# Kernel optimization log

Hardware: AMD Instinct MI355X
Metric: run time of the kernel (lower is better)

Reference implementation:

```python
import jax, jax.numpy as jnp
import numpy as np

D_MODEL = 768
N_HEADS = 12
HEAD = 64
B, T = 2, 2048


def setup_inputs() -> dict:
    key = jax.random.key(0)
    k1, k2, k3 = jax.random.split(key, 3)
    x = jax.random.normal(k1, (B, T, D_MODEL), dtype=jnp.float32)
    W1 = jax.random.normal(k2, (3 * D_MODEL, D_MODEL), dtype=jnp.float32) * (1.0 / np.sqrt(D_MODEL))
    b1 = jnp.zeros((3 * D_MODEL,), dtype=jnp.float32)
    W2 = jax.random.normal(k3, (D_MODEL, D_MODEL), dtype=jnp.float32) * (1.0 / np.sqrt(D_MODEL))
    b2 = jnp.zeros((D_MODEL,), dtype=jnp.float32)
    return {"x": x, "W1": W1, "b1": b1, "W2": W2, "b2": b2}


def reference(x, W1, b1, W2, b2):
    Bx, Tx, C = x.shape
    qkv = jnp.einsum('btc,fc->btf', x, W1) + b1            # (B,T,3C)
    q, k, v = jnp.split(qkv, 3, axis=-1)
    # (B,T,H,Dh) -> (B,H,T,Dh)
    q = q.reshape(Bx, Tx, N_HEADS, HEAD).transpose(0, 2, 1, 3)
    k = k.reshape(Bx, Tx, N_HEADS, HEAD).transpose(0, 2, 1, 3)
    v = v.reshape(Bx, Tx, N_HEADS, HEAD).transpose(0, 2, 1, 3)
    scale = 1.0 / np.sqrt(HEAD)
    scores = jnp.einsum('bhqd,bhkd->bhqk', q, k) * scale   # (B,H,T,T)
    causal = jnp.tril(jnp.ones((Tx, Tx), dtype=bool))
    scores = jnp.where(causal, scores, jnp.finfo(scores.dtype).min)
    attn = jax.nn.softmax(scores, axis=-1)
    o = jnp.einsum('bhqk,bhkd->bhqd', attn, v)             # (B,H,T,Dh)
    o = o.transpose(0, 2, 1, 3).reshape(Bx, Tx, C)
    return jnp.einsum('btc,fc->btf', o, W2) + b2
```

## Files before the change

### kernel.cpp

```cpp
#include <hip/hip_runtime.h>


typedef float f32x4 __attribute__((ext_vector_type(4)));
typedef __bf16 bf16x8 __attribute__((ext_vector_type(8)));

#define D_MODEL 768
#define F3 2304
#define NHEADS 12
#define HEAD 64
#define BB 2
#define TT 2048
#define MROWS (BB*TT)
#define KDIM 768
#define LOG2E 1.44269504f
#define NX (MROWS*D_MODEL)
#define NW1 (F3*KDIM)
#define NW2 (D_MODEL*KDIM)

__device__ __forceinline__ unsigned short f2bf(float f) {
    unsigned int u = __float_as_uint(f);
    u += 0x7fffu + ((u >> 16) & 1u);
    return (unsigned short)(u >> 16);
}
__device__ __forceinline__ unsigned int pack2bf(float a, float b) {
    unsigned int ua = __float_as_uint(a), ub = __float_as_uint(b);
    ua += 0x7fffu + ((ua >> 16) & 1u);
    ub += 0x7fffu + ((ub >> 16) & 1u);
    return (ua >> 16) | (ub & 0xffff0000u);
}

__device__ __forceinline__ void async_copy16(unsigned short* lds, const unsigned short* g) {
    __builtin_amdgcn_global_load_lds(
        (const __attribute__((address_space(1))) unsigned int*)(const void*)g,
        (__attribute__((address_space(3))) unsigned int*)(void*)lds,
        16, 0, 0);
}

__global__ void prep(const float* __restrict__ x, const float* __restrict__ W1,
                     const float* __restrict__ W2, unsigned short* __restrict__ xb,
                     unsigned short* __restrict__ w1b, unsigned short* __restrict__ w2b) {
    const int i4 = (blockIdx.x * blockDim.x + threadIdx.x) * 4;
    const float* src; unsigned short* dst; int off;
    if (i4 < NX)                { src = x;  dst = xb;  off = i4; }
    else if (i4 < NX + NW1)     { src = W1; dst = w1b; off = i4 - NX; }
    else if (i4 < NX + NW1 + NW2) { src = W2; dst = w2b; off = i4 - NX - NW1; }
    else return;
    float4 v = *(const float4*)(src + off);
    uint2 o;
    o.x = pack2bf(v.x, v.y);
    o.y = pack2bf(v.z, v.w);
    *(uint2*)(dst + off) = o;
}

__global__ __launch_bounds__(256, 4) void gemm1(
    const unsigned short* __restrict__ A, const unsigned short* __restrict__ Bw,
    const float* __restrict__ bias, int K,
    unsigned short* __restrict__ Qb, unsigned short* __restrict__ Kb,
    unsigned short* __restrict__ VT)
{
    __shared__ unsigned short As[128*64];
    __shared__ unsigned short Bs[128*64];
    const int tid  = threadIdx.x;
    const int wave = tid >> 6;
    const int lane = tid & 63;
    const int quad = lane >> 4;
    const int l16  = lane & 15;
    const int m0 = blockIdx.x * 128;
    const int n0 = blockIdx.y * 128;
    const int wm = (wave >> 1) * 64;
    const int wn = (wave & 1) * 64;

    f32x4 acc[4][4] = {};

    const unsigned short* Ablk = A + (size_t)m0 * K;
    const unsigned short* Bblk = Bw + (size_t)n0 * K;
    const int srow = (lane >> 3);
    const int scol = ((lane & 7) ^ srow) * 8;

    for (int k0 = 0; k0 < K; k0 += 64) {
        #pragma unroll
        for (int q2 = 0; q2 < 4; ++q2) {
            int t = wave * 4 + q2;
            int row = t * 8 + srow;
            async_copy16(As + t * 512, Ablk + (size_t)row * K + k0 + scol);
            async_copy16(Bs + t * 512, Bblk + (size_t)row * K + k0 + scol);
        }
        asm volatile("s_waitcnt vmcnt(0)" ::: "memory");
        __syncthreads();

        #pragma unroll
        for (int kc2 = 0; kc2 < 2; ++kc2) {
            const int pos = ((kc2*4 + quad) ^ (l16 & 7)) * 8;
            bf16x8 a[4], b[4];
            #pragma unroll
            for (int i = 0; i < 4; ++i)
                a[i] = *(const bf16x8*)(As + (wm + i*16 + l16)*64 + pos);
            #pragma unroll
            for (int j = 0; j < 4; ++j)
                b[j] = *(const bf16x8*)(Bs + (wn + j*16 + l16)*64 + pos);
            #pragma unroll
            for (int i = 0; i < 4; ++i)
                #pragma unroll
                for (int j = 0; j < 4; ++j)
                    acc[i][j] = __builtin_amdgcn_mfma_f32_16x16x32_bf16(a[i], b[j], acc[i][j], 0, 0, 0);
        }
        __syncthreads();
    }

    const int seg = blockIdx.y / 6;
    if (seg < 2) {
        #pragma unroll
        for (int j = 0; j < 4; ++j) {
            const int n = n0 + wn + j*16 + l16;
            const float bv = bias[n];
            const int f = n - seg * 768;
            const int h = f >> 6, d = f & 63;
            #pragma unroll
            for (int i = 0; i < 4; ++i)
                #pragma unroll
                for (int r = 0; r < 4; ++r) {
                    const int m = m0 + wm + i*16 + quad*4 + r;
                    const int b = m >> 11, t = m & 2047;
                    const size_t idx = (((size_t)(b*NHEADS + h)) * TT + t) * HEAD + d;
                    const float v = acc[i][j][r] + bv;
                    if (seg == 0) Qb[idx] = f2bf(v * (0.125f * LOG2E));
                    else          Kb[idx] = f2bf(v);
                }
        }
    } else {
        #pragma unroll
        for (int j = 0; j < 4; ++j) {
            const int n = n0 + wn + j*16 + l16;
            const float bv = bias[n];
            const int f = n - 1536;
            const int h = f >> 6, d = f & 63;
            #pragma unroll
            for (int i = 0; i < 4; ++i) {
                const int m = m0 + wm + i*16 + quad*4;
                const int b = m >> 11, t = m & 2047;
                uint2 pk;
                pk.x = pack2bf(acc[i][j][0] + bv, acc[i][j][1] + bv);
                pk.y = pack2bf(acc[i][j][2] + bv, acc[i][j][3] + bv);
                *(uint2*)(VT + ((size_t)(b*NHEADS + h) * HEAD + d) * TT + t) = pk;
            }
        }
    }
}

__global__ __launch_bounds__(256, 4) void gemm2(
    const unsigned short* __restrict__ A, const unsigned short* __restrict__ Bw,
    const float* __restrict__ bias, int K, float* __restrict__ Cout)
{
    __shared__ unsigned short As[64*64];
    __shared__ unsigned short Bs[128*64];
    const int tid  = threadIdx.x;
    const int wave = tid >> 6;
    const int lane = tid & 63;
    const int quad = lane >> 4;
    const int l16  = lane & 15;
    const int m0 = blockIdx.x * 64;
    const int n0 = blockIdx.y * 128;
    const int wm = (wave >> 1) * 32;
    const int wn = (wave & 1) * 64;

    f32x4 acc[2][4] = {};

    const unsigned short* Ablk = A + (size_t)m0 * K;
    const unsigned short* Bblk = Bw + (size_t)n0 * K;
    const int srow = tid >> 3;
    const int scol = ((tid & 7) ^ (srow & 7)) * 8;

    for (int k0 = 0; k0 < K; k0 += 64) {
        #pragma unroll
        for (int i = 0; i < 2; ++i)
            async_copy16(As + i*2048 + tid*8,
                         Ablk + (size_t)(i*32 + srow) * K + k0 + scol);
        #pragma unroll
        for (int i = 0; i < 4; ++i)
            async_copy16(Bs + i*2048 + tid*8,
                         Bblk + (size_t)(i*32 + srow) * K + k0 + scol);
        asm volatile("s_waitcnt vmcnt(0)" ::: "memory");
        __syncthreads();

        #pragma unroll
        for (int kc2 = 0; kc2 < 2; ++kc2) {
            const int pos = ((kc2*4 + quad) ^ (l16 & 7)) * 8;
            bf16x8 a[2], b[4];
            #pragma unroll
            for (int i = 0; i < 2; ++i)
                a[i] = *(const bf16x8*)(As + (wm + i*16 + l16)*64 + pos);
            #pragma unroll
            for (int j = 0; j < 4; ++j)
                b[j] = *(const bf16x8*)(Bs + (wn + j*16 + l16)*64 + pos);
            #pragma unroll
            for (int i = 0; i < 2; ++i)
                #pragma unroll
                for (int j = 0; j < 4; ++j)
                    acc[i][j] = __builtin_amdgcn_mfma_f32_16x16x32_bf16(a[i], b[j], acc[i][j], 0, 0, 0);
        }
        __syncthreads();
    }

    #pragma unroll
    for (int j = 0; j < 4; ++j) {
        const int n = n0 + wn + j*16 + l16;
        const float bv = bias[n];
        #pragma unroll
        for (int i = 0; i < 2; ++i)
            #pragma unroll
            for (int r = 0; r < 4; ++r) {
                const int m = m0 + wm + i*16 + quad*4 + r;
                Cout[(size_t)m * D_MODEL + n] = acc[i][j][r] + bv;
            }
    }
}

__global__ __launch_bounds__(256, 2) void attn(
    const unsigned short* __restrict__ Qb, const unsigned short* __restrict__ Kb,
    const unsigned short* __restrict__ VT, unsigned short* __restrict__ Ob)
{
    __shared__ unsigned short Ks[128*64];
    __shared__ unsigned short Vt[64*128];
    __shared__ unsigned short Ps[4][16*128];

    const int tid  = threadIdx.x;
    const int wave = tid >> 6;
    const int lane = tid & 63;
    const int quad = lane >> 4;
    const int l16  = lane & 15;
    const int qt = (blockIdx.x + blockIdx.y) & 31;
    const int bh = blockIdx.y;
    const size_t hbase = (size_t)bh * TT * HEAD;
    const int qg = qt*64 + wave*16 + l16;

    bf16x8 qreg[2];
    {
        const unsigned short* qp = Qb + hbase + (size_t)qg * HEAD + quad*8;
        qreg[0] = *(const bf16x8*)(qp);
        qreg[1] = *(const bf16x8*)(qp + 32);
    }

    const int krow = tid >> 3;
    const int kchunk = ((tid & 7) ^ (krow & 7)) * 8;
    const int vrow = tid >> 4;
    const int vchunk = ((tid & 15) ^ vrow) * 8;

    f32x4 oacc[4] = {};
    float lst = 0.f;
    const int nkt = (qt >> 1) + 1;

    for (int kt = 0; kt < nkt; ++kt) {
        __syncthreads();

        const unsigned short* ksrc = Kb + hbase + (size_t)kt * 128 * HEAD;
        #pragma unroll
        for (int i = 0; i < 4; ++i)
            async_copy16(Ks + i*2048 + tid*8,
                         ksrc + (size_t)(i*32 + krow) * 64 + kchunk);
        #pragma unroll
        for (int i = 0; i < 4; ++i)
            async_copy16(Vt + i*2048 + tid*8,
                         VT + hbase + (size_t)(i*16 + vrow) * TT + kt*128 + vchunk);
        asm volatile("s_waitcnt vmcnt(0)" ::: "memory");
        __syncthreads();

        f32x4 s[8] = {};
        #pragma unroll
        for (int kc2 = 0; kc2 < 2; ++kc2) {
            bf16x8 bq = qreg[kc2];
            const int pos = ((kc2*4 + quad) ^ (l16 & 7)) * 8;
            #pragma unroll
            for (int nt = 0; nt < 8; ++nt) {
                bf16x8 ak = *(const bf16x8*)(Ks + (nt*16 + l16)*64 + pos);
                s[nt] = __builtin_amdgcn_mfma_f32_16x16x32_bf16(ak, bq, s[nt], 0, 0, 0);
            }
        }

        if (kt == nkt - 1) {
            const int kq = kt*128 + quad*4;
            #pragma unroll
            for (int nt = 0; nt < 8; ++nt)
                #pragma unroll
                for (int r = 0; r < 4; ++r)
                    if (kq + nt*16 + r > qg) s[nt][r] = -1e30f;
        }

        float rsum = 0.f;
        uint2 pck[8];
        #pragma unroll
        for (int nt = 0; nt < 8; ++nt) {
            const float p0 = exp2f(s[nt][0]);
            const float p1 = exp2f(s[nt][1]);
            const float p2 = exp2f(s[nt][2]);
            const float p3 = exp2f(s[nt][3]);
            rsum += (p0 + p1) + (p2 + p3);
            pck[nt].x = (__float_as_uint(p0) >> 16) | (__float_as_uint(p1) & 0xffff0000u);
            pck[nt].y = (__float_as_uint(p2) >> 16) | (__float_as_uint(p3) & 0xffff0000u);
        }
        rsum += __shfl_xor(rsum, 16);
        rsum += __shfl_xor(rsum, 32);
        lst += rsum;

        #pragma unroll
        for (int nt = 0; nt < 8; ++nt)
            *(uint2*)(&Ps[wave][l16*128 + ((nt*2 + (quad>>1)) ^ l16)*8 + (quad&1)*4]) = pck[nt];

        #pragma unroll
        for (int kc = 0; kc < 4; ++kc) {
            bf16x8 ap = *(const bf16x8*)(&Ps[wave][l16*128 + ((kc*4 + quad) ^ l16)*8]);
            const int vp = ((kc*4 + quad) ^ l16) * 8;
            #pragma unroll
            for (int dt = 0; dt < 4; ++dt) {
                bf16x8 bv = *(const bf16x8*)(Vt + (dt*16 + l16)*128 + vp);
                oacc[dt] = __builtin_amdgcn_mfma_f32_16x16x32_bf16(ap, bv, oacc[dt], 0, 0, 0);
            }
        }
    }

    const float linv = 1.0f / lst;
    float lr[4];
    #pragma unroll
    for (int r = 0; r < 4; ++r) lr[r] = __shfl(linv, quad*4 + r);
    const int b = bh / NHEADS, h = bh % NHEADS;
    #pragma unroll
    for (int r = 0; r < 4; ++r) {
        const int m = b * TT + qt*64 + wave*16 + quad*4 + r;
        #pragma unroll
        for (int dt = 0; dt < 4; ++dt)
            Ob[(size_t)m * D_MODEL + h*HEAD + dt*16 + l16] = f2bf(oacc[dt][r] * lr[r]);
    }
}

extern "C" void kernel_launch(void* const* d_in, const int* in_sizes, int n_in,
                              void* d_out, int out_size, void* d_ws, size_t ws_size,
                              hipStream_t stream) {
    const float* x  = (const float*)d_in[0];
    const float* W1 = (const float*)d_in[1];
    const float* b1 = (const float*)d_in[2];
    const float* W2 = (const float*)d_in[3];
    const float* b2 = (const float*)d_in[4];
    float* out = (float*)d_out;

    unsigned short* ws = (unsigned short*)d_ws;
    unsigned short* xb  = ws;
    unsigned short* w1b = xb  + (size_t)NX;
    unsigned short* w2b = w1b + (size_t)NW1;
    unsigned short* Qb  = w2b + (size_t)NW2;
    unsigned short* Kb  = Qb + (size_t)BB*NHEADS*TT*HEAD;
    unsigned short* VT  = Kb + (size_t)BB*NHEADS*TT*HEAD;
    unsigned short* Ob  = VT + (size_t)BB*NHEADS*TT*HEAD;

    prep<<<((NX + NW1 + NW2)/4 + 255)/256, 256, 0, stream>>>(x, W1, W2, xb, w1b, w2b);

    gemm1<<<dim3(MROWS/128, F3/128), 256, 0, stream>>>(
        xb, w1b, b1, KDIM, Qb, Kb, VT);

    attn<<<dim3(32, BB*NHEADS), 256, 0, stream>>>(Qb, Kb, VT, Ob);

    gemm2<<<dim3(MROWS/64, D_MODEL/128), 256, 0, stream>>>(
        Ob, w2b, b2, KDIM, out);
}
```

Baseline: 153.4 us.

## Balance causal attention by splitting long query tiles across paired blocks

Each attention block now handles a short query tile fully plus part of a long query tile, so every block processes roughly the same number of key tiles under the causal mask. Partial numerators and row sums for long tiles are accumulated with float atomics into zeroed workspace buffers, and a new fixup kernel normalises them and writes bf16 output. This targets the load imbalance where late query tiles did far more work than early ones. The cost is extra zeroing in prep, atomic traffic, and an additional kernel launch.

```diff
diff --git a/kernel.cpp b/kernel.cpp
--- a/kernel.cpp
+++ b/kernel.cpp
@@ -16,6 +16,10 @@
 #define NX (MROWS*D_MODEL)
 #define NW1 (F3*KDIM)
 #define NW2 (D_MODEL*KDIM)
+#define NHT 16
+#define NOF (BB*NHEADS*NHT*64*64)
+#define NLF (BB*NHEADS*NHT*64)
+#define NZF (NOF+NLF)
 
 __device__ __forceinline__ unsigned short f2bf(float f) {
     unsigned int u = __float_as_uint(f);
@@ -38,12 +42,18 @@
 
 __global__ void prep(const float* __restrict__ x, const float* __restrict__ W1,
                      const float* __restrict__ W2, unsigned short* __restrict__ xb,
-                     unsigned short* __restrict__ w1b, unsigned short* __restrict__ w2b) {
+                     unsigned short* __restrict__ w1b, unsigned short* __restrict__ w2b,
+                     float* __restrict__ zf) {
     const int i4 = (blockIdx.x * blockDim.x + threadIdx.x) * 4;
     const float* src; unsigned short* dst; int off;
-    if (i4 < NX)                { src = x;  dst = xb;  off = i4; }
-    else if (i4 < NX + NW1)     { src = W1; dst = w1b; off = i4 - NX; }
+    if (i4 < NX)                  { src = x;  dst = xb;  off = i4; }
+    else if (i4 < NX + NW1)       { src = W1; dst = w1b; off = i4 - NX; }
     else if (i4 < NX + NW1 + NW2) { src = W2; dst = w2b; off = i4 - NX - NW1; }
+    else if (i4 < NX + NW1 + NW2 + NZF) {
+        f32x4 z = {};
+        *(f32x4*)(zf + (i4 - (NX + NW1 + NW2))) = z;
+        return;
+    }
     else return;
     float4 v = *(const float4*)(src + off);
     uint2 o;
@@ -217,7 +227,8 @@
 
 __global__ __launch_bounds__(256, 2) void attn(
     const unsigned short* __restrict__ Qb, const unsigned short* __restrict__ Kb,
-    const unsigned short* __restrict__ VT, unsigned short* __restrict__ Ob)
+    const unsigned short* __restrict__ VT, unsigned short* __restrict__ Ob,
+    float* __restrict__ Of, float* __restrict__ Lf)
 {
     __shared__ unsigned short Ks[128*64];
     __shared__ unsigned short Vt[64*128];
@@ -228,107 +239,163 @@
     const int lane = tid & 63;
     const int quad = lane >> 4;
     const int l16  = lane & 15;
-    const int qt = (blockIdx.x + blockIdx.y) & 31;
-    const int bh = blockIdx.y;
+    const int j    = blockIdx.x;
+    const int bh   = blockIdx.y;
+    const int i    = j & 15;
+    const bool isA = (j < 16);
+    const int half = i >> 1;
+    const int split = 8 - half;
     const size_t hbase = (size_t)bh * TT * HEAD;
-    const int qg = qt*64 + wave*16 + l16;
-
-    bf16x8 qreg[2];
-    {
-        const unsigned short* qp = Qb + hbase + (size_t)qg * HEAD + quad*8;
-        qreg[0] = *(const bf16x8*)(qp);
-        qreg[1] = *(const bf16x8*)(qp + 32);
-    }
 
     const int krow = tid >> 3;
     const int kchunk = ((tid & 7) ^ (krow & 7)) * 8;
     const int vrow = tid >> 4;
     const int vchunk = ((tid & 15) ^ vrow) * 8;
 
-    f32x4 oacc[4] = {};
-    float lst = 0.f;
-    const int nkt = (qt >> 1) + 1;
-
-    for (int kt = 0; kt < nkt; ++kt) {
-        __syncthreads();
-
-        const unsigned short* ksrc = Kb + hbase + (size_t)kt * 128 * HEAD;
-        #pragma unroll
-        for (int i = 0; i < 4; ++i)
-            async_copy16(Ks + i*2048 + tid*8,
-                         ksrc + (size_t)(i*32 + krow) * 64 + kchunk);
-        #pragma unroll
-        for (int i = 0; i < 4; ++i)
-            async_copy16(Vt + i*2048 + tid*8,
-                         VT + hbase + (size_t)(i*16 + vrow) * TT + kt*128 + vchunk);
-        asm volatile("s_waitcnt vmcnt(0)" ::: "memory");
-        __syncthreads();
-
-        f32x4 s[8] = {};
-        #pragma unroll
-        for (int kc2 = 0; kc2 < 2; ++kc2) {
-            bf16x8 bq = qreg[kc2];
-            const int pos = ((kc2*4 + quad) ^ (l16 & 7)) * 8;
+    const int nseg = isA ? 2 : 1;
+    for (int segi = 0; segi < nseg; ++segi) {
+        int qt, kb, ke; bool full;
+        if (isA) {
+            if (segi == 0) { qt = i;      kb = 0;     ke = half + 1;  full = true;  }
+            else           { qt = 31 - i; kb = 0;     ke = split;     full = false; }
+        } else             { qt = 31 - i; kb = split; ke = 16 - half; full = false; }
+        const bool domask = (ke == (qt >> 1) + 1);
+        const int qg = qt*64 + wave*16 + l16;
+
+        bf16x8 qreg[2];
+        {
+            const unsigned short* qp = Qb + hbase + (size_t)qg * HEAD + quad*8;
+            qreg[0] = *(const bf16x8*)(qp);
+            qreg[1] = *(const bf16x8*)(qp + 32);
+        }
+
+        f32x4 oacc[4] = {};
+        float lst = 0.f;
+
+        for (int kt = kb; kt < ke; ++kt) {
+            __syncthreads();
+
+            const unsigned short* ksrc = Kb + hbase + (size_t)kt * 128 * HEAD;
+            #pragma unroll
+            for (int ii = 0; ii < 4; ++ii)
+                async_copy16(Ks + ii*2048 + tid*8,
+                             ksrc + (size_t)(ii*32 + krow) * 64 + kchunk);
+            #pragma unroll
+            for (int ii = 0; ii < 4; ++ii)
+                async_copy16(Vt + ii*2048 + tid*8,
+                             VT + hbase + (size_t)(ii*16 + vrow) * TT + kt*128 + vchunk);
+            asm volatile("s_waitcnt vmcnt(0)" ::: "memory");
+            __syncthreads();
+
+            f32x4 s[8] = {};
+            #pragma unroll
+            for (int kc2 = 0; kc2 < 2; ++kc2) {
+                bf16x8 bq = qreg[kc2];
+                const int pos = ((kc2*4 + quad) ^ (l16 & 7)) * 8;
+                #pragma unroll
+                for (int nt = 0; nt < 8; ++nt) {
+                    bf16x8 ak = *(const bf16x8*)(Ks + (nt*16 + l16)*64 + pos);
+                    s[nt] = __builtin_amdgcn_mfma_f32_16x16x32_bf16(ak, bq, s[nt], 0, 0, 0);
+                }
+            }
+
+            if (domask && kt == ke - 1) {
+                const int kq = kt*128 + quad*4;
+                #pragma unroll
+                for (int nt = 0; nt < 8; ++nt)
+                    #pragma unroll
+                    for (int r = 0; r < 4; ++r)
+                        if (kq + nt*16 + r > qg) s[nt][r] = -1e30f;
+            }
+
+            float rsum = 0.f;
+            uint2 pck[8];
             #pragma unroll
             for (int nt = 0; nt < 8; ++nt) {
-                bf16x8 ak = *(const bf16x8*)(Ks + (nt*16 + l16)*64 + pos);
-                s[nt] = __builtin_amdgcn_mfma_f32_16x16x32_bf16(ak, bq, s[nt], 0, 0, 0);
-            }
-        }
-
-        if (kt == nkt - 1) {
-            const int kq = kt*128 + quad*4;
+                const float p0 = exp2f(s[nt][0]);
+                const float p1 = exp2f(s[nt][1]);
+                const float p2 = exp2f(s[nt][2]);
+                const float p3 = exp2f(s[nt][3]);
+                rsum += (p0 + p1) + (p2 + p3);
+                pck[nt].x = (__float_as_uint(p0) >> 16) | (__float_as_uint(p1) & 0xffff0000u);
+                pck[nt].y = (__float_as_uint(p2) >> 16) | (__float_as_uint(p3) & 0xffff0000u);
+            }
+            rsum += __shfl_xor(rsum, 16);
+            rsum += __shfl_xor(rsum, 32);
+            lst += rsum;
+
             #pragma unroll
             for (int nt = 0; nt < 8; ++nt)
+                *(uint2*)(&Ps[wave][l16*128 + ((nt*2 + (quad>>1)) ^ l16)*8 + (quad&1)*4]) = pck[nt];
+
+            #pragma unroll
+            for (int kc = 0; kc < 4; ++kc) {
+                bf16x8 ap = *(const bf16x8*)(&Ps[wave][l16*128 + ((kc*4 + quad) ^ l16)*8]);
+                const int vp = ((kc*4 + quad) ^ l16) * 8;
+                #pragma unroll
+                for (int dt = 0; dt < 4; ++dt) {
+                    bf16x8 bv = *(const bf16x8*)(Vt + (dt*16 + l16)*128 + vp);
+                    oacc[dt] = __builtin_amdgcn_mfma_f32_16x16x32_bf16(ap, bv, oacc[dt], 0, 0, 0);
+                }
+            }
+        }
+
+        if (full) {
+            const float linv = 1.0f / lst;
+            float lr[4];
+            #pragma unroll
+            for (int r = 0; r < 4; ++r) lr[r] = __shfl(linv, quad*4 + r);
+            const int b = bh / NHEADS, h = bh % NHEADS;
+            #pragma unroll
+            for (int r = 0; r < 4; ++r) {
+                const int m = b * TT + qt*64 + wave*16 + quad*4 + r;
+                #pragma unroll
+                for (int dt = 0; dt < 4; ++dt)
+                    Ob[(size_t)m * D_MODEL + h*HEAD + dt*16 + l16] = f2bf(oacc[dt][r] * lr[r]);
+            }
+        } else {
+            const int qtl = qt - 16;
+            float* op = Of + (((size_t)(bh*NHT + qtl))*64 + wave*16)*64;
+            #pragma unroll
+            for (int dt = 0; dt < 4; ++dt)
                 #pragma unroll
                 for (int r = 0; r < 4; ++r)
-                    if (kq + nt*16 + r > qg) s[nt][r] = -1e30f;
-        }
-
-        float rsum = 0.f;
-        uint2 pck[8];
-        #pragma unroll
-        for (int nt = 0; nt < 8; ++nt) {
-            const float p0 = exp2f(s[nt][0]);
-            const float p1 = exp2f(s[nt][1]);
-            const float p2 = exp2f(s[nt][2]);
-            const float p3 = exp2f(s[nt][3]);
-            rsum += (p0 + p1) + (p2 + p3);
-            pck[nt].x = (__float_as_uint(p0) >> 16) | (__float_as_uint(p1) & 0xffff0000u);
-            pck[nt].y = (__float_as_uint(p2) >> 16) | (__float_as_uint(p3) & 0xffff0000u);
-        }
-        rsum += __shfl_xor(rsum, 16);
-        rsum += __shfl_xor(rsum, 32);
-        lst += rsum;
-
-        #pragma unroll
-        for (int nt = 0; nt < 8; ++nt)
-            *(uint2*)(&Ps[wave][l16*128 + ((nt*2 + (quad>>1)) ^ l16)*8 + (quad&1)*4]) = pck[nt];
-
-        #pragma unroll
-        for (int kc = 0; kc < 4; ++kc) {
-            bf16x8 ap = *(const bf16x8*)(&Ps[wave][l16*128 + ((kc*4 + quad) ^ l16)*8]);
-            const int vp = ((kc*4 + quad) ^ l16) * 8;
-            #pragma unroll
-            for (int dt = 0; dt < 4; ++dt) {
-                bf16x8 bv = *(const bf16x8*)(Vt + (dt*16 + l16)*128 + vp);
-                oacc[dt] = __builtin_amdgcn_mfma_f32_16x16x32_bf16(ap, bv, oacc[dt], 0, 0, 0);
-            }
-        }
-    }
-
-    const float linv = 1.0f / lst;
-    float lr[4];
-    #pragma unroll
-    for (int r = 0; r < 4; ++r) lr[r] = __shfl(linv, quad*4 + r);
+                    atomicAdd(&op[(quad*4 + r)*64 + dt*16 + l16], oacc[dt][r]);
+            if (quad == 0)
+                atomicAdd(&Lf[((size_t)(bh*NHT + qtl))*64 + wave*16 + l16], lst);
+        }
+    }
+}
+
+__global__ __launch_bounds__(256) void fixup(
+    const float* __restrict__ Of, const float* __restrict__ Lf,
+    unsigned short* __restrict__ Ob)
+{
+    const int qtl = blockIdx.x;
+    const int bh  = blockIdx.y;
+    const int t   = threadIdx.x;
+    const int r   = t >> 2;
+    const int c0  = (t & 3) * 16;
+    const float linv = 1.0f / Lf[((size_t)(bh*NHT + qtl))*64 + r];
+    const float* src = Of + (((size_t)(bh*NHT + qtl))*64 + r)*64 + c0;
     const int b = bh / NHEADS, h = bh % NHEADS;
-    #pragma unroll
-    for (int r = 0; r < 4; ++r) {
-        const int m = b * TT + qt*64 + wave*16 + quad*4 + r;
-        #pragma unroll
-        for (int dt = 0; dt < 4; ++dt)
-            Ob[(size_t)m * D_MODEL + h*HEAD + dt*16 + l16] = f2bf(oacc[dt][r] * lr[r]);
-    }
+    const int m = b*TT + (16 + qtl)*64 + r;
+    unsigned short* dst = Ob + (size_t)m * D_MODEL + h*HEAD + c0;
+    f32x4 v0 = *(const f32x4*)(src);
+    f32x4 v1 = *(const f32x4*)(src + 4);
+    f32x4 v2 = *(const f32x4*)(src + 8);
+    f32x4 v3 = *(const f32x4*)(src + 12);
+    uint4 o0, o1;
+    o0.x = pack2bf(v0[0]*linv, v0[1]*linv);
+    o0.y = pack2bf(v0[2]*linv, v0[3]*linv);
+    o0.z = pack2bf(v1[0]*linv, v1[1]*linv);
+    o0.w = pack2bf(v1[2]*linv, v1[3]*linv);
+    o1.x = pack2bf(v2[0]*linv, v2[1]*linv);
+    o1.y = pack2bf(v2[2]*linv, v2[3]*linv);
+    o1.z = pack2bf(v3[0]*linv, v3[1]*linv);
+    o1.w = pack2bf(v3[2]*linv, v3[3]*linv);
+    *(uint4*)(dst)     = o0;
+    *(uint4*)(dst + 8) = o1;
 }
 
 extern "C" void kernel_launch(void* const* d_in, const int* in_sizes, int n_in,
@@ -349,13 +416,18 @@
     unsigned short* Kb  = Qb + (size_t)BB*NHEADS*TT*HEAD;
     unsigned short* VT  = Kb + (size_t)BB*NHEADS*TT*HEAD;
     unsigned short* Ob  = VT + (size_t)BB*NHEADS*TT*HEAD;
-
-    prep<<<((NX + NW1 + NW2)/4 + 255)/256, 256, 0, stream>>>(x, W1, W2, xb, w1b, w2b);
+    float* Of = (float*)(Ob + (size_t)NX);
+    float* Lf = Of + (size_t)NOF;
+
+    prep<<<((NX + NW1 + NW2 + NZF)/4 + 255)/256, 256, 0, stream>>>(
+        x, W1, W2, xb, w1b, w2b, Of);
 
     gemm1<<<dim3(MROWS/128, F3/128), 256, 0, stream>>>(
         xb, w1b, b1, KDIM, Qb, Kb, VT);
 
-    attn<<<dim3(32, BB*NHEADS), 256, 0, stream>>>(Qb, Kb, VT, Ob);
+    attn<<<dim3(32, BB*NHEADS), 256, 0, stream>>>(Qb, Kb, VT, Ob, Of, Lf);
+
+    fixup<<<dim3(NHT, BB*NHEADS), 256, 0, stream>>>(Of, Lf, Ob);
 
     gemm2<<<dim3(MROWS/64, D_MODEL/128), 256, 0, stream>>>(
         Ob, w2b, b2, KDIM, out);
```

Result: no change. 152.1 us (-0.8%).
